# Kernel tuning notes

Hardware: AMD Instinct MI355X
Metric: run time of the kernel (lower is better)

The kernel has to match this reference:

```python
import jax, jax.numpy as jnp
import numpy as np

STRIDES = (8, 16, 32, 64, 128)
TOPK = 1000          # fixed candidate count (jit-friendly stand-in for boolean masking)
SCORE_TH = 0.05      # from `score > 0.05` in postProcessing
IOU_TH = 0.5         # standard FCOS NMS threshold


def _decode_level(cls, cnt, reg, stride):
    # cls [B,C,H,W], cnt [B,1,H,W], reg [B,4,H,W]
    B, C, H, W = cls.shape
    p_cls = jax.nn.sigmoid(cls).transpose(0, 2, 3, 1).reshape(B, H * W, C)
    p_cnt = jax.nn.sigmoid(cnt).transpose(0, 2, 3, 1).reshape(B, H * W, 1)
    p_reg = jnp.exp(reg).transpose(0, 2, 3, 1).reshape(B, H * W, 4)  # (l,t,r,b) distances
    ys = (jnp.arange(H, dtype=cls.dtype) + 0.5) * stride
    xs = (jnp.arange(W, dtype=cls.dtype) + 0.5) * stride
    yy, xx = jnp.meshgrid(ys, xs, indexing='ij')
    cx = xx.reshape(-1)[None, :]  # [1,HW]
    cy = yy.reshape(-1)[None, :]
    boxes = jnp.stack([cx - p_reg[..., 0], cy - p_reg[..., 1],
                       cx + p_reg[..., 2], cy + p_reg[..., 3]], axis=-1)  # [B,HW,4]
    return p_cls, p_cnt, boxes


def _iou_matrix(b):
    # b [K,4] (x1,y1,x2,y2) -> [K,K]
    area = jnp.clip(b[:, 2] - b[:, 0], 0) * jnp.clip(b[:, 3] - b[:, 1], 0)
    x1 = jnp.maximum(b[:, None, 0], b[None, :, 0])
    y1 = jnp.maximum(b[:, None, 1], b[None, :, 1])
    x2 = jnp.minimum(b[:, None, 2], b[None, :, 2])
    y2 = jnp.minimum(b[:, None, 3], b[None, :, 3])
    inter = jnp.clip(x2 - x1, 0) * jnp.clip(y2 - y1, 0)
    return inter / (area[:, None] + area[None, :] - inter + 1e-9)


def _nms_keep(boxes, scores):
    # boxes [K,4] sorted by descending score, scores [K] -> keep mask [K]
    K = boxes.shape[0]
    iou = _iou_matrix(boxes)
    idx = jnp.arange(K)
    keep0 = scores > SCORE_TH
    def body(i, keep):
        sup = (iou[i] > IOU_TH) & (idx > i) & keep[i]
        return keep & ~sup
    return jax.lax.fori_loop(0, K, body, keep0)


def _detect(levels):
    cls_l, cnt_l, box_l = [], [], []
    for (c, n, r), s in zip(levels, STRIDES):
        pc, pn, pb = _decode_level(c, n, r, s)
        cls_l.append(pc); cnt_l.append(pn); box_l.append(pb)
    cls = jnp.concatenate(cls_l, 1)    # [B,N,C]
    boxes = jnp.concatenate(box_l, 1)  # [B,N,4]
    score = cls.max(-1)                # per original: score from cls (cnt unused in score)
    kind = cls.argmax(-1)
    top_s, top_i = jax.lax.top_k(score, TOPK)                      # [B,K]
    top_b = jnp.take_along_axis(boxes, top_i[..., None], axis=1)   # [B,K,4]
    top_k = jnp.take_along_axis(kind, top_i, axis=1)               # [B,K]
    keep = jax.vmap(_nms_keep)(top_b, top_s)                       # [B,K] bool
    out = jnp.concatenate([top_b,
                           top_k[..., None].astype(cls.dtype),
                           top_s[..., None],
                           keep[..., None].astype(cls.dtype)], axis=-1)  # [B,K,7]
    return out


def setup_inputs() -> dict:
    key = jax.random.key(0)
    B, C = 16, 20
    hw = [(128, 160), (64, 80), (32, 40), (16, 20), (8, 10)]
    names = []
    for p in (3, 4, 5, 6, 7):
        names += [f'cls_p{p}', f'cnt_p{p}', f'reg_p{p}']
    ks = jax.random.split(key, len(names))
    inp = {}
    for li, (H, W) in enumerate(hw):
        inp[f'cls_p{li+3}'] = jax.random.normal(ks[3*li+0], (B, C, H, W), jnp.float32)
        inp[f'cnt_p{li+3}'] = jax.random.normal(ks[3*li+1], (B, 1, H, W), jnp.float32)
        inp[f'reg_p{li+3}'] = jax.random.normal(ks[3*li+2], (B, 4, H, W), jnp.float32)
    return inp


def reference(cls_p3, cnt_p3, reg_p3, cls_p4, cnt_p4, reg_p4,
              cls_p5, cnt_p5, reg_p5, cls_p6, cnt_p6, reg_p6,
              cls_p7, cnt_p7, reg_p7):
    levels = [(cls_p3, cnt_p3, reg_p3), (cls_p4, cnt_p4, reg_p4),
              (cls_p5, cnt_p5, reg_p5), (cls_p6, cnt_p6, reg_p6),
              (cls_p7, cnt_p7, reg_p7)]
    return _detect(levels)
```

## Files before the change

kernel.cpp:

```cpp
#include <hip/hip_runtime.h>
#include <math.h>

#define BATCH 16
#define NCH 20
#define NPOS 27280
#define NTOP 1000
#define KW 16
#define NBIN 4096
#define CANDCAP 4096
#define NSLICE 14
#define SLICEPOS 2048

typedef unsigned long long u64;
typedef unsigned int u32;

__device__ __align__(16) u32 g_sb[BATCH * NPOS];
__device__ unsigned char g_kind[BATCH * NPOS];
__device__ u32 g_hph[BATCH * NSLICE * NBIN];
__device__ u32 g_suf[BATCH * NBIN];
__device__ u32 g_cnt[BATCH * NBIN];
__device__ u32 g_dcnt[BATCH * NBIN];
__device__ int g_thr[BATCH];
__device__ int g_ncand[BATCH];
__device__ u64 g_cand[BATCH * CANDCAP];
__device__ float4 g_box[BATCH * NTOP];
__device__ float g_score[BATCH * NTOP];
__device__ u64 g_maskT[BATCH * KW * NTOP];
__device__ unsigned char g_rowsup[BATCH * NTOP];

__device__ __forceinline__ int digit_of(u32 sb) {
  int d = ((int)sb - 0x3F000000) >> 11;
  return d < 0 ? 0 : (d > (NBIN - 1) ? (NBIN - 1) : d);
}

__device__ __forceinline__ int jj(int j) { return j + (j >> 6); }
#define SKEWCAP (NTOP + NTOP / 64 + 1)

__global__ __launch_bounds__(1024) void k1_score(
    const float* __restrict__ c3, const float* __restrict__ c4,
    const float* __restrict__ c5, const float* __restrict__ c6,
    const float* __restrict__ c7) {
  int b = blockIdx.y, bx = blockIdx.x, tid = threadIdx.x;
  __shared__ u32 lh[NBIN];
  for (int j = tid; j < NBIN; j += 1024) lh[j] = 0;
  __syncthreads();

  int n0 = bx * SLICEPOS + tid * 2;
  if (n0 < NPOS) {
    const float* cls; int off, hw;
    if (n0 < 20480)      { cls = c3; off = 0;     hw = 20480; }
    else if (n0 < 25600) { cls = c4; off = 20480; hw = 5120;  }
    else if (n0 < 26880) { cls = c5; off = 25600; hw = 1280;  }
    else if (n0 < 27200) { cls = c6; off = 26880; hw = 320;   }
    else                 { cls = c7; off = 27200; hw = 80;    }
    int local = n0 - off;
    const float2* p = (const float2*)(cls + (size_t)b * NCH * hw + local);
    int s2 = hw >> 1;
    float2 best = p[0];
    int k0 = 0, k1 = 0;
    for (int c = 1; c < NCH; ++c) {
      float2 v = p[(size_t)c * s2];
      if (v.x > best.x) { best.x = v.x; k0 = c; }
      if (v.y > best.y) { best.y = v.y; k1 = c; }
    }
    float bb[2] = {best.x, best.y};
    u32 sb[2];
#pragma unroll
    for (int i = 0; i < 2; ++i) {
      float e = (float)exp(-(double)bb[i]);
      float s = 1.0f / (1.0f + e);
      sb[i] = __float_as_uint(s);
      atomicAdd(&lh[digit_of(sb[i])], 1u);
    }
    uint2 sb2; sb2.x = sb[0]; sb2.y = sb[1];
    *(uint2*)&g_sb[(size_t)b * NPOS + n0] = sb2;
    *(unsigned short*)&g_kind[(size_t)b * NPOS + n0] =
        (unsigned short)((u32)k0 | ((u32)k1 << 8));
  }
  __syncthreads();
  u32* ph = g_hph + ((size_t)b * NSLICE + bx) * NBIN;
  for (int j = tid; j < NBIN; j += 1024) ph[j] = lh[j];
}

__global__ __launch_bounds__(1024) void k2_scan() {
  int b = blockIdx.x, tid = threadIdx.x;
  int lane = tid & 63, wid = tid >> 6;
  __shared__ u32 wsum[16];
  u32 c[4];
#pragma unroll
  for (int k = 0; k < 4; ++k) {
    int d = 4 * tid + k;
    u32 s = 0;
    for (int p = 0; p < NSLICE; ++p) s += g_hph[((size_t)b * NSLICE + p) * NBIN + d];
    c[k] = s;
    g_cnt[b * NBIN + d] = s;
  }
  u32 tot = c[0] + c[1] + c[2] + c[3];
  u32 s = tot;
#pragma unroll
  for (int off = 1; off < 64; off <<= 1) {
    u32 v = __shfl_down(s, off);
    if (lane + off < 64) s += v;
  }
  if (lane == 0) wsum[wid] = s;
  __syncthreads();
  u32 wexcl = 0;
  for (int w2 = wid + 1; w2 < 16; ++w2) wexcl += wsum[w2];
  u32 e = wexcl + (s - tot);
  u32 e3 = e;
  u32 e2 = e3 + c[3];
  u32 e1 = e2 + c[2];
  u32 e0 = e1 + c[1];
  g_suf[b * NBIN + 4 * tid + 3] = e3;
  g_suf[b * NBIN + 4 * tid + 2] = e2;
  g_suf[b * NBIN + 4 * tid + 1] = e1;
  g_suf[b * NBIN + 4 * tid + 0] = e0;
  if (e3 < NTOP && NTOP <= e3 + c[3]) { g_thr[b] = 4 * tid + 3; g_ncand[b] = (int)(e3 + c[3]); }
  if (e2 < NTOP && NTOP <= e2 + c[2]) { g_thr[b] = 4 * tid + 2; g_ncand[b] = (int)(e2 + c[2]); }
  if (e1 < NTOP && NTOP <= e1 + c[1]) { g_thr[b] = 4 * tid + 1; g_ncand[b] = (int)(e1 + c[1]); }
  if (e0 < NTOP && NTOP <= e0 + c[0]) { g_thr[b] = 4 * tid + 0; g_ncand[b] = (int)(e0 + c[0]); }
  for (int j = tid; j < NBIN; j += 1024) g_dcnt[b * NBIN + j] = 0;
}

__global__ __launch_bounds__(1024) void k3_compact() {
  int b = blockIdx.y, bx = blockIdx.x, tid = threadIdx.x;
  int n0 = bx * SLICEPOS + tid * 2;
  if (n0 >= NPOS) return;
  int thr = g_thr[b];
  uint2 sb2 = *(const uint2*)&g_sb[(size_t)b * NPOS + n0];
  u32 sb[2] = {sb2.x, sb2.y};
#pragma unroll
  for (int i = 0; i < 2; ++i) {
    int d = digit_of(sb[i]);
    if (d >= thr) {
      u32 slot = g_suf[b * NBIN + d] + atomicAdd(&g_dcnt[b * NBIN + d], 1u);
      if (slot < CANDCAP)
        g_cand[b * CANDCAP + slot] = ((u64)sb[i] << 15) | (u32)(NPOS - (n0 + i));
    }
  }
}

__global__ __launch_bounds__(256) void k4_rank(
    const float* __restrict__ r3, const float* __restrict__ r4,
    const float* __restrict__ r5, const float* __restrict__ r6,
    const float* __restrict__ r7, float* __restrict__ out) {
  int b = blockIdx.y, bx = blockIdx.x, tid = threadIdx.x;
  int ncand = g_ncand[b];
  if (ncand > CANDCAP) ncand = CANDCAP;
  for (int i = bx * 256 + tid; i < ncand; i += 8 * 256) {
    u64 k = g_cand[b * CANDCAP + i];
    int d = digit_of((u32)(k >> 15));
    u32 gs = g_suf[b * NBIN + d];
    u32 ge = gs + g_cnt[b * NBIN + d];
    if (ge > (u32)ncand) ge = (u32)ncand;
    int rank = (int)gs;
    for (u32 j = gs; j < ge; ++j) rank += (int)(g_cand[b * CANDCAP + j] > k);
    if (rank >= NTOP) continue;
    u32 n = (u32)NPOS - (u32)(k & 0x7FFFu);
    float sc = __uint_as_float((u32)(k >> 15));
    const float* reg; int off, hw, lvl;
    if (n < 20480)      { reg = r3; off = 0;     hw = 20480; lvl = 0; }
    else if (n < 25600) { reg = r4; off = 20480; hw = 5120;  lvl = 1; }
    else if (n < 26880) { reg = r5; off = 25600; hw = 1280;  lvl = 2; }
    else if (n < 27200) { reg = r6; off = 26880; hw = 320;   lvl = 3; }
    else                { reg = r7; off = 27200; hw = 80;    lvl = 4; }
    int local = (int)n - off;
    int W = 160 >> lvl;
    int hh = local / W, ww = local - hh * W;
    float stride = (float)(8 << lvl);
    const float* rp = reg + (size_t)b * 4 * hw + local;
    float e0 = expf(rp[0]);
    float e1 = expf(rp[(size_t)hw]);
    float e2 = expf(rp[(size_t)2 * hw]);
    float e3 = expf(rp[(size_t)3 * hw]);
    float cx = (ww + 0.5f) * stride, cy = (hh + 0.5f) * stride;
    float x1 = cx - e0, y1 = cy - e1, x2 = cx + e2, y2 = cy + e3;
    int ok = b * NTOP + rank;
    g_box[ok] = make_float4(x1, y1, x2, y2);
    g_score[ok] = sc;
    float* o = out + (size_t)ok * 7;
    o[0] = x1; o[1] = y1; o[2] = x2; o[3] = y2;
    o[4] = (float)g_kind[(size_t)b * NPOS + n];
    o[5] = sc;
  }
}

__global__ __launch_bounds__(256) void k5_mask() {
  int b = blockIdx.y;
  int ig = blockIdx.x;
  int tid = threadIdx.x;
  int lane = tid & 63;
  int jlo = ig * 16;
  int nst = NTOP - jlo;
  __shared__ float4 shbox[SKEWCAP];
  __shared__ float shA[SKEWCAP];
  const float4* boxes = g_box + b * NTOP;
  for (int j = tid; j < nst; j += 256) {
    float4 bj = boxes[jlo + j];
    shbox[jj(j)] = bj;
    shA[jj(j)] = fmaxf(bj.z - bj.x, 0.f) * fmaxf(bj.w - bj.y, 0.f);
  }
  __syncthreads();
  int i = jlo + (tid >> 4);
  int t = tid & 15;
  u64 word = 0;
  if (i < NTOP) {
    float4 bi = shbox[jj(i - jlo)];
    float aarea = shA[jj(i - jlo)];
    int j0 = t * 64;
    int jbeg = (j0 > i + 1) ? j0 : i + 1;
    int jend = (j0 + 64 < NTOP) ? j0 + 64 : NTOP;
    for (int j = jbeg; j < jend; ++j) {
      float4 bj = shbox[jj(j - jlo)];
      float barea = shA[jj(j - jlo)];
      float ix1 = fmaxf(bi.x, bj.x), iy1 = fmaxf(bi.y, bj.y);
      float ix2 = fminf(bi.z, bj.z), iy2 = fminf(bi.w, bj.w);
      float inter = fmaxf(ix2 - ix1, 0.f) * fmaxf(iy2 - iy1, 0.f);
      if (inter + inter > aarea + barea - inter + 1e-9f)
        word |= 1ull << (j - j0);
    }
    g_maskT[((size_t)b * KW + t) * NTOP + i] = word;
  }
  u64 b16 = __ballot(word != 0);
  int rg = lane >> 4;
  if (t == 0 && i < NTOP)
    g_rowsup[b * NTOP + i] = (unsigned char)(((b16 >> (rg * 16)) & 0xFFFFull) ? 1 : 0);
}

__global__ __launch_bounds__(64) void k6_greedy(float* __restrict__ out) {
  int b = blockIdx.x;
  int lane = threadIdx.x;
  int col = lane & 15, g = lane >> 4;
  const u64* maskT = g_maskT + (size_t)b * KW * NTOP;

  u64 mdiag[KW];
  float s[KW];
  unsigned char rs[KW];
#pragma unroll
  for (int w = 0; w < KW; ++w) {
    int k = w * 64 + lane;
    mdiag[w] = (k < NTOP) ? maskT[(size_t)w * NTOP + k] : 0ull;
    s[w] = (k < NTOP) ? g_score[b * NTOP + k] : 0.f;
    rs[w] = (k < NTOP) ? g_rowsup[b * NTOP + k] : (unsigned char)0;
  }

  u64 remv = 0;
  for (int w = 0; w < KW; ++w) {
    int k = w * 64 + lane;
    u64 keep0 = __ballot(k < NTOP && s[w] > 0.05f);
    u64 gate = __ballot(rs[w] != 0);
    u64 cur = keep0 & ~__shfl(remv, w);
    u64 rem = cur & gate;
    u64 acc = 0;
    while (rem) {
      int i = __ffsll(rem) - 1;
      u64 v = __shfl(mdiag[w], i);
      rem &= ~(v | (1ull << i));
      cur &= ~v;
      acc |= (1ull << i);
    }
    u64 upd = 0;
#pragma unroll
    for (int r = 0; r < 16; ++r) {
      int i2 = g * 16 + r;
      if ((acc >> i2) & 1ull) {
        int row = w * 64 + i2;
        if (row < NTOP) upd |= maskT[(size_t)col * NTOP + row];
      }
    }
    upd |= __shfl_xor(upd, 16);
    upd |= __shfl_xor(upd, 32);
    remv |= upd;
    if (k < NTOP) out[(size_t)(b * NTOP + k) * 7 + 6] = (float)((cur >> lane) & 1ull);
  }
}

extern "C" void kernel_launch(void* const* d_in, const int* in_sizes, int n_in,
                              void* d_out, int out_size, void* d_ws, size_t ws_size,
                              hipStream_t stream) {
  const float* c3 = (const float*)d_in[0];
  const float* r3 = (const float*)d_in[2];
  const float* c4 = (const float*)d_in[3];
  const float* r4 = (const float*)d_in[5];
  const float* c5 = (const float*)d_in[6];
  const float* r5 = (const float*)d_in[8];
  const float* c6 = (const float*)d_in[9];
  const float* r6 = (const float*)d_in[11];
  const float* c7 = (const float*)d_in[12];
  const float* r7 = (const float*)d_in[14];
  float* out = (float*)d_out;

  hipLaunchKernelGGL(k1_score, dim3(NSLICE, BATCH), dim3(1024), 0, stream,
                     c3, c4, c5, c6, c7);
  hipLaunchKernelGGL(k2_scan, dim3(BATCH), dim3(1024), 0, stream);
  hipLaunchKernelGGL(k3_compact, dim3(NSLICE, BATCH), dim3(1024), 0, stream);
  hipLaunchKernelGGL(k4_rank, dim3(8, BATCH), dim3(256), 0, stream,
                     r3, r4, r5, r6, r7, out);
  hipLaunchKernelGGL(k5_mask, dim3(63, BATCH), dim3(256), 0, stream);
  hipLaunchKernelGGL(k6_greedy, dim3(BATCH), dim3(64), 0, stream, out);
}
```

Before: 58.01 us.

## Fuse six NMS pipeline kernels into one cooperative persistent kernel with grid syncs

Merges the score/histogram, scan, compact, rank, IoU-mask and greedy NMS kernels into a single cooperative kernel of 224 blocks of 1024 threads, separated by grid.sync barriers. This removes five kernel launch boundaries and their inter-kernel gaps. The mask stage is remapped to 1024-thread blocks covering 64 rows each, and the greedy stage runs on one wavefront per batch while the other threads idle. Grid-wide barriers cost something, and the large blocks with shared memory for all stages may limit co-residency.

```diff
diff --git a/kernel.cpp b/kernel.cpp
--- a/kernel.cpp
+++ b/kernel.cpp
@@ -1,5 +1,8 @@
 #include <hip/hip_runtime.h>
+#include <hip/hip_cooperative_groups.h>
 #include <math.h>
+
+namespace cg = cooperative_groups;
 
 #define BATCH 16
 #define NCH 20
@@ -10,6 +13,7 @@
 #define CANDCAP 4096
 #define NSLICE 14
 #define SLICEPOS 2048
+#define GRID (NSLICE * BATCH)
 
 typedef unsigned long long u64;
 typedef unsigned int u32;
@@ -36,242 +40,251 @@
 __device__ __forceinline__ int jj(int j) { return j + (j >> 6); }
 #define SKEWCAP (NTOP + NTOP / 64 + 1)
 
-__global__ __launch_bounds__(1024) void k1_score(
+__global__ __launch_bounds__(1024, 4) void fcos_fused(
     const float* __restrict__ c3, const float* __restrict__ c4,
     const float* __restrict__ c5, const float* __restrict__ c6,
-    const float* __restrict__ c7) {
-  int b = blockIdx.y, bx = blockIdx.x, tid = threadIdx.x;
-  __shared__ u32 lh[NBIN];
-  for (int j = tid; j < NBIN; j += 1024) lh[j] = 0;
-  __syncthreads();
-
-  int n0 = bx * SLICEPOS + tid * 2;
-  if (n0 < NPOS) {
-    const float* cls; int off, hw;
-    if (n0 < 20480)      { cls = c3; off = 0;     hw = 20480; }
-    else if (n0 < 25600) { cls = c4; off = 20480; hw = 5120;  }
-    else if (n0 < 26880) { cls = c5; off = 25600; hw = 1280;  }
-    else if (n0 < 27200) { cls = c6; off = 26880; hw = 320;   }
-    else                 { cls = c7; off = 27200; hw = 80;    }
-    int local = n0 - off;
-    const float2* p = (const float2*)(cls + (size_t)b * NCH * hw + local);
-    int s2 = hw >> 1;
-    float2 best = p[0];
-    int k0 = 0, k1 = 0;
-    for (int c = 1; c < NCH; ++c) {
-      float2 v = p[(size_t)c * s2];
-      if (v.x > best.x) { best.x = v.x; k0 = c; }
-      if (v.y > best.y) { best.y = v.y; k1 = c; }
-    }
-    float bb[2] = {best.x, best.y};
-    u32 sb[2];
-#pragma unroll
-    for (int i = 0; i < 2; ++i) {
-      float e = (float)exp(-(double)bb[i]);
-      float s = 1.0f / (1.0f + e);
-      sb[i] = __float_as_uint(s);
-      atomicAdd(&lh[digit_of(sb[i])], 1u);
-    }
-    uint2 sb2; sb2.x = sb[0]; sb2.y = sb[1];
-    *(uint2*)&g_sb[(size_t)b * NPOS + n0] = sb2;
-    *(unsigned short*)&g_kind[(size_t)b * NPOS + n0] =
-        (unsigned short)((u32)k0 | ((u32)k1 << 8));
-  }
-  __syncthreads();
-  u32* ph = g_hph + ((size_t)b * NSLICE + bx) * NBIN;
-  for (int j = tid; j < NBIN; j += 1024) ph[j] = lh[j];
-}
-
-__global__ __launch_bounds__(1024) void k2_scan() {
-  int b = blockIdx.x, tid = threadIdx.x;
-  int lane = tid & 63, wid = tid >> 6;
-  __shared__ u32 wsum[16];
-  u32 c[4];
-#pragma unroll
-  for (int k = 0; k < 4; ++k) {
-    int d = 4 * tid + k;
-    u32 s = 0;
-    for (int p = 0; p < NSLICE; ++p) s += g_hph[((size_t)b * NSLICE + p) * NBIN + d];
-    c[k] = s;
-    g_cnt[b * NBIN + d] = s;
-  }
-  u32 tot = c[0] + c[1] + c[2] + c[3];
-  u32 s = tot;
-#pragma unroll
-  for (int off = 1; off < 64; off <<= 1) {
-    u32 v = __shfl_down(s, off);
-    if (lane + off < 64) s += v;
-  }
-  if (lane == 0) wsum[wid] = s;
-  __syncthreads();
-  u32 wexcl = 0;
-  for (int w2 = wid + 1; w2 < 16; ++w2) wexcl += wsum[w2];
-  u32 e = wexcl + (s - tot);
-  u32 e3 = e;
-  u32 e2 = e3 + c[3];
-  u32 e1 = e2 + c[2];
-  u32 e0 = e1 + c[1];
-  g_suf[b * NBIN + 4 * tid + 3] = e3;
-  g_suf[b * NBIN + 4 * tid + 2] = e2;
-  g_suf[b * NBIN + 4 * tid + 1] = e1;
-  g_suf[b * NBIN + 4 * tid + 0] = e0;
-  if (e3 < NTOP && NTOP <= e3 + c[3]) { g_thr[b] = 4 * tid + 3; g_ncand[b] = (int)(e3 + c[3]); }
-  if (e2 < NTOP && NTOP <= e2 + c[2]) { g_thr[b] = 4 * tid + 2; g_ncand[b] = (int)(e2 + c[2]); }
-  if (e1 < NTOP && NTOP <= e1 + c[1]) { g_thr[b] = 4 * tid + 1; g_ncand[b] = (int)(e1 + c[1]); }
-  if (e0 < NTOP && NTOP <= e0 + c[0]) { g_thr[b] = 4 * tid + 0; g_ncand[b] = (int)(e0 + c[0]); }
-  for (int j = tid; j < NBIN; j += 1024) g_dcnt[b * NBIN + j] = 0;
-}
-
-__global__ __launch_bounds__(1024) void k3_compact() {
-  int b = blockIdx.y, bx = blockIdx.x, tid = threadIdx.x;
-  int n0 = bx * SLICEPOS + tid * 2;
-  if (n0 >= NPOS) return;
-  int thr = g_thr[b];
-  uint2 sb2 = *(const uint2*)&g_sb[(size_t)b * NPOS + n0];
-  u32 sb[2] = {sb2.x, sb2.y};
-#pragma unroll
-  for (int i = 0; i < 2; ++i) {
-    int d = digit_of(sb[i]);
-    if (d >= thr) {
-      u32 slot = g_suf[b * NBIN + d] + atomicAdd(&g_dcnt[b * NBIN + d], 1u);
-      if (slot < CANDCAP)
-        g_cand[b * CANDCAP + slot] = ((u64)sb[i] << 15) | (u32)(NPOS - (n0 + i));
-    }
-  }
-}
-
-__global__ __launch_bounds__(256) void k4_rank(
+    const float* __restrict__ c7,
     const float* __restrict__ r3, const float* __restrict__ r4,
     const float* __restrict__ r5, const float* __restrict__ r6,
     const float* __restrict__ r7, float* __restrict__ out) {
-  int b = blockIdx.y, bx = blockIdx.x, tid = threadIdx.x;
-  int ncand = g_ncand[b];
-  if (ncand > CANDCAP) ncand = CANDCAP;
-  for (int i = bx * 256 + tid; i < ncand; i += 8 * 256) {
-    u64 k = g_cand[b * CANDCAP + i];
-    int d = digit_of((u32)(k >> 15));
-    u32 gs = g_suf[b * NBIN + d];
-    u32 ge = gs + g_cnt[b * NBIN + d];
-    if (ge > (u32)ncand) ge = (u32)ncand;
-    int rank = (int)gs;
-    for (u32 j = gs; j < ge; ++j) rank += (int)(g_cand[b * CANDCAP + j] > k);
-    if (rank >= NTOP) continue;
-    u32 n = (u32)NPOS - (u32)(k & 0x7FFFu);
-    float sc = __uint_as_float((u32)(k >> 15));
-    const float* reg; int off, hw, lvl;
-    if (n < 20480)      { reg = r3; off = 0;     hw = 20480; lvl = 0; }
-    else if (n < 25600) { reg = r4; off = 20480; hw = 5120;  lvl = 1; }
-    else if (n < 26880) { reg = r5; off = 25600; hw = 1280;  lvl = 2; }
-    else if (n < 27200) { reg = r6; off = 26880; hw = 320;   lvl = 3; }
-    else                { reg = r7; off = 27200; hw = 80;    lvl = 4; }
-    int local = (int)n - off;
-    int W = 160 >> lvl;
-    int hh = local / W, ww = local - hh * W;
-    float stride = (float)(8 << lvl);
-    const float* rp = reg + (size_t)b * 4 * hw + local;
-    float e0 = expf(rp[0]);
-    float e1 = expf(rp[(size_t)hw]);
-    float e2 = expf(rp[(size_t)2 * hw]);
-    float e3 = expf(rp[(size_t)3 * hw]);
-    float cx = (ww + 0.5f) * stride, cy = (hh + 0.5f) * stride;
-    float x1 = cx - e0, y1 = cy - e1, x2 = cx + e2, y2 = cy + e3;
-    int ok = b * NTOP + rank;
-    g_box[ok] = make_float4(x1, y1, x2, y2);
-    g_score[ok] = sc;
-    float* o = out + (size_t)ok * 7;
-    o[0] = x1; o[1] = y1; o[2] = x2; o[3] = y2;
-    o[4] = (float)g_kind[(size_t)b * NPOS + n];
-    o[5] = sc;
-  }
-}
-
-__global__ __launch_bounds__(256) void k5_mask() {
-  int b = blockIdx.y;
-  int ig = blockIdx.x;
+  cg::grid_group grid = cg::this_grid();
+  int blk = blockIdx.x;
   int tid = threadIdx.x;
-  int lane = tid & 63;
-  int jlo = ig * 16;
-  int nst = NTOP - jlo;
+  int lane = tid & 63, wid = tid >> 6;
+
+  __shared__ u32 lh[NBIN];
   __shared__ float4 shbox[SKEWCAP];
   __shared__ float shA[SKEWCAP];
-  const float4* boxes = g_box + b * NTOP;
-  for (int j = tid; j < nst; j += 256) {
-    float4 bj = boxes[jlo + j];
-    shbox[jj(j)] = bj;
-    shA[jj(j)] = fmaxf(bj.z - bj.x, 0.f) * fmaxf(bj.w - bj.y, 0.f);
-  }
-  __syncthreads();
-  int i = jlo + (tid >> 4);
-  int t = tid & 15;
-  u64 word = 0;
-  if (i < NTOP) {
-    float4 bi = shbox[jj(i - jlo)];
-    float aarea = shA[jj(i - jlo)];
-    int j0 = t * 64;
-    int jbeg = (j0 > i + 1) ? j0 : i + 1;
-    int jend = (j0 + 64 < NTOP) ? j0 + 64 : NTOP;
-    for (int j = jbeg; j < jend; ++j) {
-      float4 bj = shbox[jj(j - jlo)];
-      float barea = shA[jj(j - jlo)];
-      float ix1 = fmaxf(bi.x, bj.x), iy1 = fmaxf(bi.y, bj.y);
-      float ix2 = fminf(bi.z, bj.z), iy2 = fminf(bi.w, bj.w);
-      float inter = fmaxf(ix2 - ix1, 0.f) * fmaxf(iy2 - iy1, 0.f);
-      if (inter + inter > aarea + barea - inter + 1e-9f)
-        word |= 1ull << (j - j0);
-    }
-    g_maskT[((size_t)b * KW + t) * NTOP + i] = word;
-  }
-  u64 b16 = __ballot(word != 0);
-  int rg = lane >> 4;
-  if (t == 0 && i < NTOP)
-    g_rowsup[b * NTOP + i] = (unsigned char)(((b16 >> (rg * 16)) & 0xFFFFull) ? 1 : 0);
-}
-
-__global__ __launch_bounds__(64) void k6_greedy(float* __restrict__ out) {
-  int b = blockIdx.x;
-  int lane = threadIdx.x;
-  int col = lane & 15, g = lane >> 4;
-  const u64* maskT = g_maskT + (size_t)b * KW * NTOP;
-
-  u64 mdiag[KW];
-  float s[KW];
-  unsigned char rs[KW];
-#pragma unroll
-  for (int w = 0; w < KW; ++w) {
-    int k = w * 64 + lane;
-    mdiag[w] = (k < NTOP) ? maskT[(size_t)w * NTOP + k] : 0ull;
-    s[w] = (k < NTOP) ? g_score[b * NTOP + k] : 0.f;
-    rs[w] = (k < NTOP) ? g_rowsup[b * NTOP + k] : (unsigned char)0;
-  }
-
-  u64 remv = 0;
-  for (int w = 0; w < KW; ++w) {
-    int k = w * 64 + lane;
-    u64 keep0 = __ballot(k < NTOP && s[w] > 0.05f);
-    u64 gate = __ballot(rs[w] != 0);
-    u64 cur = keep0 & ~__shfl(remv, w);
-    u64 rem = cur & gate;
-    u64 acc = 0;
-    while (rem) {
-      int i = __ffsll(rem) - 1;
-      u64 v = __shfl(mdiag[w], i);
-      rem &= ~(v | (1ull << i));
-      cur &= ~v;
-      acc |= (1ull << i);
-    }
-    u64 upd = 0;
-#pragma unroll
-    for (int r = 0; r < 16; ++r) {
-      int i2 = g * 16 + r;
-      if ((acc >> i2) & 1ull) {
-        int row = w * 64 + i2;
-        if (row < NTOP) upd |= maskT[(size_t)col * NTOP + row];
-      }
-    }
-    upd |= __shfl_xor(upd, 16);
-    upd |= __shfl_xor(upd, 32);
-    remv |= upd;
-    if (k < NTOP) out[(size_t)(b * NTOP + k) * 7 + 6] = (float)((cur >> lane) & 1ull);
+  __shared__ u32 wsum[16];
+
+  {
+    int b = blk / NSLICE, bx = blk % NSLICE;
+    for (int j = tid; j < NBIN; j += 1024) lh[j] = 0;
+    __syncthreads();
+    int n0 = bx * SLICEPOS + tid * 2;
+    if (n0 < NPOS) {
+      const float* cls; int off, hw;
+      if (n0 < 20480)      { cls = c3; off = 0;     hw = 20480; }
+      else if (n0 < 25600) { cls = c4; off = 20480; hw = 5120;  }
+      else if (n0 < 26880) { cls = c5; off = 25600; hw = 1280;  }
+      else if (n0 < 27200) { cls = c6; off = 26880; hw = 320;   }
+      else                 { cls = c7; off = 27200; hw = 80;    }
+      int local = n0 - off;
+      const float2* p = (const float2*)(cls + (size_t)b * NCH * hw + local);
+      int s2 = hw >> 1;
+      float2 best = p[0];
+      int k0 = 0, k1 = 0;
+      for (int c = 1; c < NCH; ++c) {
+        float2 v = p[(size_t)c * s2];
+        if (v.x > best.x) { best.x = v.x; k0 = c; }
+        if (v.y > best.y) { best.y = v.y; k1 = c; }
+      }
+      float bb[2] = {best.x, best.y};
+      u32 sb[2];
+#pragma unroll
+      for (int i = 0; i < 2; ++i) {
+        float e = (float)exp(-(double)bb[i]);
+        float s = 1.0f / (1.0f + e);
+        sb[i] = __float_as_uint(s);
+        atomicAdd(&lh[digit_of(sb[i])], 1u);
+      }
+      uint2 sb2; sb2.x = sb[0]; sb2.y = sb[1];
+      *(uint2*)&g_sb[(size_t)b * NPOS + n0] = sb2;
+      *(unsigned short*)&g_kind[(size_t)b * NPOS + n0] =
+          (unsigned short)((u32)k0 | ((u32)k1 << 8));
+    }
+    __syncthreads();
+    u32* ph = g_hph + ((size_t)b * NSLICE + bx) * NBIN;
+    for (int j = tid; j < NBIN; j += 1024) ph[j] = lh[j];
+  }
+  grid.sync();
+
+  if (blk < BATCH) {
+    int b = blk;
+    u32 c[4];
+#pragma unroll
+    for (int k = 0; k < 4; ++k) {
+      int d = 4 * tid + k;
+      u32 s = 0;
+      for (int p = 0; p < NSLICE; ++p) s += g_hph[((size_t)b * NSLICE + p) * NBIN + d];
+      c[k] = s;
+      g_cnt[b * NBIN + d] = s;
+    }
+    u32 tot = c[0] + c[1] + c[2] + c[3];
+    u32 s = tot;
+#pragma unroll
+    for (int off = 1; off < 64; off <<= 1) {
+      u32 v = __shfl_down(s, off);
+      if (lane + off < 64) s += v;
+    }
+    if (lane == 0) wsum[wid] = s;
+    __syncthreads();
+    u32 wexcl = 0;
+    for (int w2 = wid + 1; w2 < 16; ++w2) wexcl += wsum[w2];
+    u32 e = wexcl + (s - tot);
+    u32 e3 = e;
+    u32 e2 = e3 + c[3];
+    u32 e1 = e2 + c[2];
+    u32 e0 = e1 + c[1];
+    g_suf[b * NBIN + 4 * tid + 3] = e3;
+    g_suf[b * NBIN + 4 * tid + 2] = e2;
+    g_suf[b * NBIN + 4 * tid + 1] = e1;
+    g_suf[b * NBIN + 4 * tid + 0] = e0;
+    if (e3 < NTOP && NTOP <= e3 + c[3]) { g_thr[b] = 4 * tid + 3; g_ncand[b] = (int)(e3 + c[3]); }
+    if (e2 < NTOP && NTOP <= e2 + c[2]) { g_thr[b] = 4 * tid + 2; g_ncand[b] = (int)(e2 + c[2]); }
+    if (e1 < NTOP && NTOP <= e1 + c[1]) { g_thr[b] = 4 * tid + 1; g_ncand[b] = (int)(e1 + c[1]); }
+    if (e0 < NTOP && NTOP <= e0 + c[0]) { g_thr[b] = 4 * tid + 0; g_ncand[b] = (int)(e0 + c[0]); }
+    for (int j = tid; j < NBIN; j += 1024) g_dcnt[b * NBIN + j] = 0;
+  }
+  grid.sync();
+
+  {
+    int b = blk / NSLICE, bx = blk % NSLICE;
+    int n0 = bx * SLICEPOS + tid * 2;
+    if (n0 < NPOS) {
+      int thr = g_thr[b];
+      uint2 sb2 = *(const uint2*)&g_sb[(size_t)b * NPOS + n0];
+      u32 sb[2] = {sb2.x, sb2.y};
+#pragma unroll
+      for (int i = 0; i < 2; ++i) {
+        int d = digit_of(sb[i]);
+        if (d >= thr) {
+          u32 slot = g_suf[b * NBIN + d] + atomicAdd(&g_dcnt[b * NBIN + d], 1u);
+          if (slot < CANDCAP)
+            g_cand[b * CANDCAP + slot] = ((u64)sb[i] << 15) | (u32)(NPOS - (n0 + i));
+        }
+      }
+    }
+  }
+  grid.sync();
+
+  {
+    int b = blk / NSLICE, sub = blk % NSLICE;
+    int ncand = g_ncand[b];
+    if (ncand > CANDCAP) ncand = CANDCAP;
+    for (int i = sub * 1024 + tid; i < ncand; i += NSLICE * 1024) {
+      u64 k = g_cand[b * CANDCAP + i];
+      int d = digit_of((u32)(k >> 15));
+      u32 gs = g_suf[b * NBIN + d];
+      u32 ge = gs + g_cnt[b * NBIN + d];
+      if (ge > (u32)ncand) ge = (u32)ncand;
+      int rank = (int)gs;
+      for (u32 j = gs; j < ge; ++j) rank += (int)(g_cand[b * CANDCAP + j] > k);
+      if (rank >= NTOP) continue;
+      u32 n = (u32)NPOS - (u32)(k & 0x7FFFu);
+      float sc = __uint_as_float((u32)(k >> 15));
+      const float* reg; int off, hw, lvl;
+      if (n < 20480)      { reg = r3; off = 0;     hw = 20480; lvl = 0; }
+      else if (n < 25600) { reg = r4; off = 20480; hw = 5120;  lvl = 1; }
+      else if (n < 26880) { reg = r5; off = 25600; hw = 1280;  lvl = 2; }
+      else if (n < 27200) { reg = r6; off = 26880; hw = 320;   lvl = 3; }
+      else                { reg = r7; off = 27200; hw = 80;    lvl = 4; }
+      int local = (int)n - off;
+      int W = 160 >> lvl;
+      int hh = local / W, ww = local - hh * W;
+      float stride = (float)(8 << lvl);
+      const float* rp = reg + (size_t)b * 4 * hw + local;
+      float e0 = expf(rp[0]);
+      float e1 = expf(rp[(size_t)hw]);
+      float e2 = expf(rp[(size_t)2 * hw]);
+      float e3 = expf(rp[(size_t)3 * hw]);
+      float cx = (ww + 0.5f) * stride, cy = (hh + 0.5f) * stride;
+      float x1 = cx - e0, y1 = cy - e1, x2 = cx + e2, y2 = cy + e3;
+      int ok = b * NTOP + rank;
+      g_box[ok] = make_float4(x1, y1, x2, y2);
+      g_score[ok] = sc;
+      float* o = out + (size_t)ok * 7;
+      o[0] = x1; o[1] = y1; o[2] = x2; o[3] = y2;
+      o[4] = (float)g_kind[(size_t)b * NPOS + n];
+      o[5] = sc;
+    }
+  }
+  grid.sync();
+
+  for (int u = blk; u < BATCH * 16; u += GRID) {
+    int b = u >> 4, ig = u & 15;
+    int jlo = ig * 64;
+    int nst = NTOP - jlo;
+    __syncthreads();
+    const float4* boxes = g_box + b * NTOP;
+    for (int j = tid; j < nst; j += 1024) {
+      float4 bj = boxes[jlo + j];
+      shbox[jj(j)] = bj;
+      shA[jj(j)] = fmaxf(bj.z - bj.x, 0.f) * fmaxf(bj.w - bj.y, 0.f);
+    }
+    __syncthreads();
+    int i = jlo + (tid >> 4);
+    int t = tid & 15;
+    u64 word = 0;
+    if (i < NTOP) {
+      float4 bi = shbox[jj(i - jlo)];
+      float aarea = shA[jj(i - jlo)];
+      int j0 = t * 64;
+      int jbeg = (j0 > i + 1) ? j0 : i + 1;
+      int jend = (j0 + 64 < NTOP) ? j0 + 64 : NTOP;
+      for (int j = jbeg; j < jend; ++j) {
+        float4 bj = shbox[jj(j - jlo)];
+        float barea = shA[jj(j - jlo)];
+        float ix1 = fmaxf(bi.x, bj.x), iy1 = fmaxf(bi.y, bj.y);
+        float ix2 = fminf(bi.z, bj.z), iy2 = fminf(bi.w, bj.w);
+        float inter = fmaxf(ix2 - ix1, 0.f) * fmaxf(iy2 - iy1, 0.f);
+        if (inter + inter > aarea + barea - inter + 1e-9f)
+          word |= 1ull << (j - j0);
+      }
+      g_maskT[((size_t)b * KW + t) * NTOP + i] = word;
+    }
+    u64 b16 = __ballot(word != 0);
+    int rg = lane >> 4;
+    if (t == 0 && i < NTOP)
+      g_rowsup[b * NTOP + i] = (unsigned char)(((b16 >> (rg * 16)) & 0xFFFFull) ? 1 : 0);
+  }
+  grid.sync();
+
+  if (blk < BATCH && tid < 64) {
+    int b = blk;
+    int col = lane & 15, g = lane >> 4;
+    const u64* maskT = g_maskT + (size_t)b * KW * NTOP;
+
+    u64 mdiag[KW];
+    float s[KW];
+    unsigned char rs[KW];
+#pragma unroll
+    for (int w = 0; w < KW; ++w) {
+      int k = w * 64 + lane;
+      mdiag[w] = (k < NTOP) ? maskT[(size_t)w * NTOP + k] : 0ull;
+      s[w] = (k < NTOP) ? g_score[b * NTOP + k] : 0.f;
+      rs[w] = (k < NTOP) ? g_rowsup[b * NTOP + k] : (unsigned char)0;
+    }
+
+    u64 remv = 0;
+    for (int w = 0; w < KW; ++w) {
+      int k = w * 64 + lane;
+      u64 keep0 = __ballot(k < NTOP && s[w] > 0.05f);
+      u64 gate = __ballot(rs[w] != 0);
+      u64 cur = keep0 & ~__shfl(remv, w);
+      u64 rem = cur & gate;
+      u64 acc = 0;
+      while (rem) {
+        int i = __ffsll(rem) - 1;
+        u64 v = __shfl(mdiag[w], i);
+        rem &= ~(v | (1ull << i));
+        cur &= ~v;
+        acc |= (1ull << i);
+      }
+      u64 upd = 0;
+#pragma unroll
+      for (int r = 0; r < 16; ++r) {
+        int i2 = g * 16 + r;
+        if ((acc >> i2) & 1ull) {
+          int row = w * 64 + i2;
+          if (row < NTOP) upd |= maskT[(size_t)col * NTOP + row];
+        }
+      }
+      upd |= __shfl_xor(upd, 16);
+      upd |= __shfl_xor(upd, 32);
+      remv |= upd;
+      if (k < NTOP) out[(size_t)(b * NTOP + k) * 7 + 6] = (float)((cur >> lane) & 1ull);
+    }
   }
 }
 
@@ -290,12 +303,9 @@
   const float* r7 = (const float*)d_in[14];
   float* out = (float*)d_out;
 
-  hipLaunchKernelGGL(k1_score, dim3(NSLICE, BATCH), dim3(1024), 0, stream,
-                     c3, c4, c5, c6, c7);
-  hipLaunchKernelGGL(k2_scan, dim3(BATCH), dim3(1024), 0, stream);
-  hipLaunchKernelGGL(k3_compact, dim3(NSLICE, BATCH), dim3(1024), 0, stream);
-  hipLaunchKernelGGL(k4_rank, dim3(8, BATCH), dim3(256), 0, stream,
-                     r3, r4, r5, r6, r7, out);
-  hipLaunchKernelGGL(k5_mask, dim3(63, BATCH), dim3(256), 0, stream);
-  hipLaunchKernelGGL(k6_greedy, dim3(BATCH), dim3(64), 0, stream, out);
+  void* args[] = {(void*)&c3, (void*)&c4, (void*)&c5, (void*)&c6, (void*)&c7,
+                  (void*)&r3, (void*)&r4, (void*)&r5, (void*)&r6, (void*)&r7,
+                  (void*)&out};
+  hipLaunchCooperativeKernel((const void*)fcos_fused, dim3(GRID), dim3(1024),
+                             args, 0, stream);
 }
```

Result: slower. 203.8 us (+251.2%).

## Fuse histogram scan into compaction kernel and vectorize score pass to float4

Applied to the files above, without the earlier changes.

Removes the separate k2_scan launch. Every k3_compact block now recomputes the per-batch histogram suffix scan into shared memory, and block 0 writes g_cnt, g_suf and g_ncand for later kernels. The g_dcnt zeroing moves into k1_score, and k1 switches to 512 threads handling 4 positions each with float4 loads. The cost is 14x redundant scan work per batch in place of one launch plus a global round trip. Zeroing g_dcnt in k1 is safe because k1 finishes before k3 starts.

```diff
diff --git a/kernel.cpp b/kernel.cpp
--- a/kernel.cpp
+++ b/kernel.cpp
@@ -20,7 +20,6 @@
 __device__ u32 g_suf[BATCH * NBIN];
 __device__ u32 g_cnt[BATCH * NBIN];
 __device__ u32 g_dcnt[BATCH * NBIN];
-__device__ int g_thr[BATCH];
 __device__ int g_ncand[BATCH];
 __device__ u64 g_cand[BATCH * CANDCAP];
 __device__ float4 g_box[BATCH * NTOP];
@@ -36,16 +35,19 @@
 __device__ __forceinline__ int jj(int j) { return j + (j >> 6); }
 #define SKEWCAP (NTOP + NTOP / 64 + 1)
 
-__global__ __launch_bounds__(1024) void k1_score(
+__global__ __launch_bounds__(512) void k1_score(
     const float* __restrict__ c3, const float* __restrict__ c4,
     const float* __restrict__ c5, const float* __restrict__ c6,
     const float* __restrict__ c7) {
   int b = blockIdx.y, bx = blockIdx.x, tid = threadIdx.x;
   __shared__ u32 lh[NBIN];
-  for (int j = tid; j < NBIN; j += 1024) lh[j] = 0;
-  __syncthreads();
-
-  int n0 = bx * SLICEPOS + tid * 2;
+  for (int j = tid; j < NBIN; j += 512) lh[j] = 0;
+  int blkflat = b * NSLICE + bx;
+  int z = blkflat * 512 + tid;
+  if (z < BATCH * NBIN) g_dcnt[z] = 0;
+  __syncthreads();
+
+  int n0 = bx * SLICEPOS + tid * 4;
   if (n0 < NPOS) {
     const float* cls; int off, hw;
     if (n0 < 20480)      { cls = c3; off = 0;     hw = 20480; }
@@ -54,38 +56,43 @@
     else if (n0 < 27200) { cls = c6; off = 26880; hw = 320;   }
     else                 { cls = c7; off = 27200; hw = 80;    }
     int local = n0 - off;
-    const float2* p = (const float2*)(cls + (size_t)b * NCH * hw + local);
-    int s2 = hw >> 1;
-    float2 best = p[0];
-    int k0 = 0, k1 = 0;
+    const float4* p = (const float4*)(cls + (size_t)b * NCH * hw + local);
+    int s4 = hw >> 2;
+    float4 best = p[0];
+    int k0 = 0, k1 = 0, k2 = 0, k3 = 0;
     for (int c = 1; c < NCH; ++c) {
-      float2 v = p[(size_t)c * s2];
+      float4 v = p[(size_t)c * s4];
       if (v.x > best.x) { best.x = v.x; k0 = c; }
       if (v.y > best.y) { best.y = v.y; k1 = c; }
-    }
-    float bb[2] = {best.x, best.y};
-    u32 sb[2];
-#pragma unroll
-    for (int i = 0; i < 2; ++i) {
+      if (v.z > best.z) { best.z = v.z; k2 = c; }
+      if (v.w > best.w) { best.w = v.w; k3 = c; }
+    }
+    float bb[4] = {best.x, best.y, best.z, best.w};
+    u32 sb[4];
+#pragma unroll
+    for (int i = 0; i < 4; ++i) {
       float e = (float)exp(-(double)bb[i]);
       float s = 1.0f / (1.0f + e);
       sb[i] = __float_as_uint(s);
       atomicAdd(&lh[digit_of(sb[i])], 1u);
     }
-    uint2 sb2; sb2.x = sb[0]; sb2.y = sb[1];
-    *(uint2*)&g_sb[(size_t)b * NPOS + n0] = sb2;
-    *(unsigned short*)&g_kind[(size_t)b * NPOS + n0] =
-        (unsigned short)((u32)k0 | ((u32)k1 << 8));
+    uint4 sb4; sb4.x = sb[0]; sb4.y = sb[1]; sb4.z = sb[2]; sb4.w = sb[3];
+    *(uint4*)&g_sb[(size_t)b * NPOS + n0] = sb4;
+    u32 kind4 = (u32)k0 | ((u32)k1 << 8) | ((u32)k2 << 16) | ((u32)k3 << 24);
+    *(u32*)&g_kind[(size_t)b * NPOS + n0] = kind4;
   }
   __syncthreads();
   u32* ph = g_hph + ((size_t)b * NSLICE + bx) * NBIN;
-  for (int j = tid; j < NBIN; j += 1024) ph[j] = lh[j];
-}
-
-__global__ __launch_bounds__(1024) void k2_scan() {
-  int b = blockIdx.x, tid = threadIdx.x;
+  for (int j = tid; j < NBIN; j += 512) ph[j] = lh[j];
+}
+
+__global__ __launch_bounds__(1024) void k3_compact() {
+  int b = blockIdx.y, bx = blockIdx.x, tid = threadIdx.x;
   int lane = tid & 63, wid = tid >> 6;
+  __shared__ u32 suf[NBIN];
   __shared__ u32 wsum[16];
+  __shared__ int sh_thr;
+
   u32 c[4];
 #pragma unroll
   for (int k = 0; k < 4; ++k) {
@@ -93,7 +100,6 @@
     u32 s = 0;
     for (int p = 0; p < NSLICE; ++p) s += g_hph[((size_t)b * NSLICE + p) * NBIN + d];
     c[k] = s;
-    g_cnt[b * NBIN + d] = s;
   }
   u32 tot = c[0] + c[1] + c[2] + c[3];
   u32 s = tot;
@@ -111,31 +117,39 @@
   u32 e2 = e3 + c[3];
   u32 e1 = e2 + c[2];
   u32 e0 = e1 + c[1];
-  g_suf[b * NBIN + 4 * tid + 3] = e3;
-  g_suf[b * NBIN + 4 * tid + 2] = e2;
-  g_suf[b * NBIN + 4 * tid + 1] = e1;
-  g_suf[b * NBIN + 4 * tid + 0] = e0;
-  if (e3 < NTOP && NTOP <= e3 + c[3]) { g_thr[b] = 4 * tid + 3; g_ncand[b] = (int)(e3 + c[3]); }
-  if (e2 < NTOP && NTOP <= e2 + c[2]) { g_thr[b] = 4 * tid + 2; g_ncand[b] = (int)(e2 + c[2]); }
-  if (e1 < NTOP && NTOP <= e1 + c[1]) { g_thr[b] = 4 * tid + 1; g_ncand[b] = (int)(e1 + c[1]); }
-  if (e0 < NTOP && NTOP <= e0 + c[0]) { g_thr[b] = 4 * tid + 0; g_ncand[b] = (int)(e0 + c[0]); }
-  for (int j = tid; j < NBIN; j += 1024) g_dcnt[b * NBIN + j] = 0;
-}
-
-__global__ __launch_bounds__(1024) void k3_compact() {
-  int b = blockIdx.y, bx = blockIdx.x, tid = threadIdx.x;
+  suf[4 * tid + 3] = e3;
+  suf[4 * tid + 2] = e2;
+  suf[4 * tid + 1] = e1;
+  suf[4 * tid + 0] = e0;
+  if (e3 < NTOP && NTOP <= e3 + c[3]) { sh_thr = 4 * tid + 3; if (bx == 0) g_ncand[b] = (int)(e3 + c[3]); }
+  if (e2 < NTOP && NTOP <= e2 + c[2]) { sh_thr = 4 * tid + 2; if (bx == 0) g_ncand[b] = (int)(e2 + c[2]); }
+  if (e1 < NTOP && NTOP <= e1 + c[1]) { sh_thr = 4 * tid + 1; if (bx == 0) g_ncand[b] = (int)(e1 + c[1]); }
+  if (e0 < NTOP && NTOP <= e0 + c[0]) { sh_thr = 4 * tid + 0; if (bx == 0) g_ncand[b] = (int)(e0 + c[0]); }
+  if (bx == 0) {
+#pragma unroll
+    for (int k = 0; k < 4; ++k) {
+      g_cnt[b * NBIN + 4 * tid + k] = c[k];
+    }
+    g_suf[b * NBIN + 4 * tid + 0] = e0;
+    g_suf[b * NBIN + 4 * tid + 1] = e1;
+    g_suf[b * NBIN + 4 * tid + 2] = e2;
+    g_suf[b * NBIN + 4 * tid + 3] = e3;
+  }
+  __syncthreads();
+  int thr = sh_thr;
+
   int n0 = bx * SLICEPOS + tid * 2;
-  if (n0 >= NPOS) return;
-  int thr = g_thr[b];
-  uint2 sb2 = *(const uint2*)&g_sb[(size_t)b * NPOS + n0];
-  u32 sb[2] = {sb2.x, sb2.y};
-#pragma unroll
-  for (int i = 0; i < 2; ++i) {
-    int d = digit_of(sb[i]);
-    if (d >= thr) {
-      u32 slot = g_suf[b * NBIN + d] + atomicAdd(&g_dcnt[b * NBIN + d], 1u);
-      if (slot < CANDCAP)
-        g_cand[b * CANDCAP + slot] = ((u64)sb[i] << 15) | (u32)(NPOS - (n0 + i));
+  if (n0 < NPOS) {
+    uint2 sb2 = *(const uint2*)&g_sb[(size_t)b * NPOS + n0];
+    u32 sb[2] = {sb2.x, sb2.y};
+#pragma unroll
+    for (int i = 0; i < 2; ++i) {
+      int d = digit_of(sb[i]);
+      if (d >= thr) {
+        u32 slot = suf[d] + atomicAdd(&g_dcnt[b * NBIN + d], 1u);
+        if (slot < CANDCAP)
+          g_cand[b * CANDCAP + slot] = ((u64)sb[i] << 15) | (u32)(NPOS - (n0 + i));
+      }
     }
   }
 }
@@ -290,9 +304,8 @@
   const float* r7 = (const float*)d_in[14];
   float* out = (float*)d_out;
 
-  hipLaunchKernelGGL(k1_score, dim3(NSLICE, BATCH), dim3(1024), 0, stream,
+  hipLaunchKernelGGL(k1_score, dim3(NSLICE, BATCH), dim3(512), 0, stream,
                      c3, c4, c5, c6, c7);
-  hipLaunchKernelGGL(k2_scan, dim3(BATCH), dim3(1024), 0, stream);
   hipLaunchKernelGGL(k3_compact, dim3(NSLICE, BATCH), dim3(1024), 0, stream);
   hipLaunchKernelGGL(k4_rank, dim3(8, BATCH), dim3(256), 0, stream,
                      r3, r4, r5, r6, r7, out);
```

Measured after the change: 60.53 us. 4.3% more time.
